# Kernel tuning notes

Hardware: AMD Instinct MI355X
Metric: run time of the kernel (lower is better)

The kernel has to match this reference:

```python
import jax, jax.numpy as jnp
import numpy as np

# Llama-7B-like decode-step config (GQA)
H = 32      # query heads
HKV = 8     # kv heads
D = 128     # head dim
HID = 4096  # hidden size (= H*D)
S = 32768   # stored quantized cache length
B = 1       # batch
Q = 1       # q_len (fused SmartKV path requires q_len == 1)


def rotate_half(x):
    return jnp.concatenate([-x[..., D // 2:], x[..., :D // 2]], axis=-1)


def setup_inputs() -> dict:
    key = jax.random.key(0)
    ks = jax.random.split(key, 9)
    hidden_states = jax.random.normal(ks[0], (B, Q, HID), jnp.float32)
    # quantized KV cache: signed int codes + per-(token, kv_head) scales
    k_qx = jax.random.randint(ks[1], (S, HKV, D), -128, 128, jnp.int32)
    v_qx = jax.random.randint(ks[2], (S, HKV, D), -128, 128, jnp.int32)
    k_scale = jax.random.uniform(ks[3], (S, HKV, 1), jnp.float32, 0.005, 0.02)
    v_scale = jax.random.uniform(ks[4], (S, HKV, 1), jnp.float32, 0.005, 0.02)
    # RoPE angles for the current decode position (pos = S)
    inv_freq = 1.0 / (10000.0 ** (jnp.arange(0, D, 2).astype(jnp.float32) / D))
    ang = jnp.concatenate([S * inv_freq, S * inv_freq])  # [D]
    cos = jnp.cos(ang)
    sin = jnp.sin(ang)
    sc = 1.0 / np.sqrt(HID)
    Wq = jax.random.normal(ks[5], (HID, H * D), jnp.float32) * sc
    Wk = jax.random.normal(ks[6], (HID, HKV * D), jnp.float32) * sc
    Wv = jax.random.normal(ks[7], (HID, HKV * D), jnp.float32) * sc
    Wo = jax.random.normal(ks[8], (H * D, HID), jnp.float32) * sc
    return dict(hidden_states=hidden_states, k_qx=k_qx, k_scale=k_scale,
                v_qx=v_qx, v_scale=v_scale, cos=cos, sin=sin,
                Wq=Wq, Wk=Wk, Wv=Wv, Wo=Wo)


def reference(hidden_states, k_qx, k_scale, v_qx, v_scale, cos, sin, Wq, Wk, Wv, Wo):
    b, q_len, _ = hidden_states.shape  # b=1, q_len=1 (decode)
    G = H // HKV  # GQA group size
    # QKV projections
    q = (hidden_states @ Wq).reshape(b, q_len, H, D).transpose(0, 2, 1, 3)      # [B,H,Q,D]
    k = (hidden_states @ Wk).reshape(b, q_len, HKV, D).transpose(0, 2, 1, 3)    # [B,HKV,Q,D]
    v = (hidden_states @ Wv).reshape(b, q_len, HKV, D).transpose(0, 2, 1, 3)    # [B,HKV,Q,D]
    # RoPE on current-token q, k
    c = cos[None, None, None, :]
    s = sin[None, None, None, :]
    q = q * c + rotate_half(q) * s
    k = k * c + rotate_half(k) * s
    # inline dequantization of SmartKV cache (kept at HKV heads; GQA handled in einsum
    # instead of materializing repeat_interleave)
    Kp = k_qx.astype(jnp.float32) * k_scale  # [S,HKV,D]
    Vp = v_qx.astype(jnp.float32) * v_scale  # [S,HKV,D]
    qg = q.reshape(b, HKV, G, q_len, D)
    scale = 1.0 / jnp.sqrt(jnp.float32(D))
    s_past = jnp.einsum('bkgqd,skd->bkgqs', qg, Kp) * scale        # [B,HKV,G,Q,S]
    s_cur = jnp.einsum('bkgqd,bkqd->bkgq', qg, k)[..., None] * scale  # current token
    scores = jnp.concatenate([s_past, s_cur], axis=-1)             # [B,HKV,G,Q,S+1]
    probs = jax.nn.softmax(scores, axis=-1)
    out = (jnp.einsum('bkgqs,skd->bkgqd', probs[..., :S], Vp)
           + probs[..., S:] * v[:, :, None, :, :])                 # [B,HKV,G,Q,D]
    out = out.reshape(b, H, q_len, D).transpose(0, 2, 1, 3).reshape(b, q_len, H * D)
    return out @ Wo
```

## Files before the change

### kernel.cpp

```cpp
#include <hip/hip_runtime.h>
#include <hip/hip_bf16.h>

#define H_    32
#define HKV_  8
#define D_    128
#define HID_  4096
#define NQKV  6144
#define SPLIT 128
#define CHUNK 256
#define S_    32768
#define NCHUNK (S_ / CHUNK)
#define SCALE_ 0.08838834764831843f
#define BASE_  8.0f

#define WS_QKV_PART 0
#define WS_QKV      786432
#define WS_PV_C     792576
#define WS_L_C      1316864
#define WS_ATTN     1320960
#define WS_OPART    1325056

__global__ __launch_bounds__(256) void k_qkv_part(
    const float* __restrict__ hid, const float* __restrict__ Wq,
    const float* __restrict__ Wk, const float* __restrict__ Wv,
    float* __restrict__ part)
{
    const int j0 = blockIdx.x * 1024 + threadIdx.x * 4;
    const int i0 = blockIdx.y * (HID_ / SPLIT);
    __shared__ float hs[HID_ / SPLIT];
    if (threadIdx.x < HID_ / SPLIT) hs[threadIdx.x] = hid[i0 + threadIdx.x];
    __syncthreads();

    const float* W; int ldw; int col;
    if (j0 < 4096)       { W = Wq; ldw = 4096; col = j0; }
    else if (j0 < 5120)  { W = Wk; ldw = 1024; col = j0 - 4096; }
    else                 { W = Wv; ldw = 1024; col = j0 - 5120; }

    float4 acc = {0.f, 0.f, 0.f, 0.f};
    const float* p = W + (size_t)i0 * ldw + col;
    #pragma unroll 8
    for (int i = 0; i < HID_ / SPLIT; ++i) {
        const float4 wv = *(const float4*)(p + (size_t)i * ldw);
        const float h = hs[i];
        acc.x += h * wv.x; acc.y += h * wv.y; acc.z += h * wv.z; acc.w += h * wv.w;
    }
    *(float4*)&part[(size_t)blockIdx.y * NQKV + j0] = acc;
}

__global__ __launch_bounds__(256) void k_qkv_reduce(
    const float* __restrict__ part, const float* __restrict__ cosv,
    const float* __restrict__ sinv, float* __restrict__ qkv)
{
    const int j = blockIdx.x * 256 + threadIdx.x;
    float s = 0.f;
    #pragma unroll 8
    for (int k = 0; k < SPLIT; ++k) s += part[(size_t)k * NQKV + j];
    __shared__ float buf[256];
    buf[threadIdx.x] = s;
    __syncthreads();
    float out = s;
    if (j < 5120) {
        const int d = j & 127;
        const float rot = (d < 64) ? -buf[threadIdx.x + 64] : buf[threadIdx.x - 64];
        out = s * cosv[d] + rot * sinv[d];
    }
    qkv[j] = out;
}

__global__ __launch_bounds__(256) void k_attn(
    const int* __restrict__ kqx, const float* __restrict__ kscale,
    const int* __restrict__ vqx, const float* __restrict__ vscale,
    const float* __restrict__ qkv, float* __restrict__ pv_c,
    float* __restrict__ l_c)
{
    const int kh = blockIdx.y;
    const int c0 = blockIdx.x * CHUNK;
    const int tid = threadIdx.x;
    const int g = tid >> 6;
    const int l = tid & 63;
    const int t = l >> 3, j = l & 7;

    float4 qf[4];
    #pragma unroll
    for (int k = 0; k < 4; ++k)
        qf[k] = *(const float4*)&qkv[(kh * 4 + g) * D_ + (j + 8 * k) * 4];

    float ls = 0.f;
    float4 acc[4];
    #pragma unroll
    for (int k = 0; k < 4; ++k) acc[k] = make_float4(0.f, 0.f, 0.f, 0.f);

    #pragma unroll 2
    for (int it = 0; it < CHUNK / 8; ++it) {
        const int tok = c0 + it * 8 + t;
        const size_t row = ((size_t)tok * HKV_ + kh) * D_;
        int4 kv[4], vv[4];
        #pragma unroll
        for (int k = 0; k < 4; ++k) kv[k] = *(const int4*)(kqx + row + (j + 8 * k) * 4);
        #pragma unroll
        for (int k = 0; k < 4; ++k) vv[k] = *(const int4*)(vqx + row + (j + 8 * k) * 4);
        const float sc = kscale[tok * HKV_ + kh] * SCALE_;
        const float vs = vscale[tok * HKV_ + kh];

        float dot = 0.f;
        #pragma unroll
        for (int k = 0; k < 4; ++k)
            dot += (float)kv[k].x * qf[k].x + (float)kv[k].y * qf[k].y +
                   (float)kv[k].z * qf[k].z + (float)kv[k].w * qf[k].w;
        dot += __shfl_xor(dot, 1, 64);
        dot += __shfl_xor(dot, 2, 64);
        dot += __shfl_xor(dot, 4, 64);

        const float wgt = __expf(dot * sc - BASE_);
        ls += wgt;
        const float wv = wgt * vs;
        #pragma unroll
        for (int k = 0; k < 4; ++k) {
            acc[k].x += wv * (float)vv[k].x;
            acc[k].y += wv * (float)vv[k].y;
            acc[k].z += wv * (float)vv[k].z;
            acc[k].w += wv * (float)vv[k].w;
        }
    }

    #pragma unroll
    for (int msk = 8; msk < 64; msk <<= 1) {
        #pragma unroll
        for (int k = 0; k < 4; ++k) {
            acc[k].x += __shfl_xor(acc[k].x, msk, 64);
            acc[k].y += __shfl_xor(acc[k].y, msk, 64);
            acc[k].z += __shfl_xor(acc[k].z, msk, 64);
            acc[k].w += __shfl_xor(acc[k].w, msk, 64);
        }
        ls += __shfl_xor(ls, msk, 64);
    }
    if (t == 0) {
        float* dst = pv_c + ((size_t)(blockIdx.x * HKV_ + kh) * 4 + g) * D_;
        #pragma unroll
        for (int k = 0; k < 4; ++k) *(float4*)(dst + (j + 8 * k) * 4) = acc[k];
        if (j == 0) l_c[(blockIdx.x * HKV_ + kh) * 4 + g] = ls;
    }
}

__global__ __launch_bounds__(128) void k_combine(
    const float* __restrict__ pv_c, const float* __restrict__ l_c,
    const float* __restrict__ qkv, float* __restrict__ attn)
{
    const int h = blockIdx.x;
    const int d = threadIdx.x;
    const int kh = h >> 2, g = h & 3;

    __shared__ float sred[128];
    sred[d] = qkv[h * D_ + d] * qkv[4096 + kh * D_ + d];
    __syncthreads();
    for (int s2 = 64; s2 > 0; s2 >>= 1) {
        if (d < s2) sred[d] += sred[d + s2];
        __syncthreads();
    }
    const float pc = __expf(sred[0] * SCALE_ - BASE_);

    float pv = 0.f, dsum = 0.f;
    for (int c = 0; c < NCHUNK; ++c) {
        pv   += pv_c[((size_t)(c * HKV_ + kh) * 4 + g) * D_ + d];
        dsum += l_c[(c * HKV_ + kh) * 4 + g];
    }
    const float vcur = qkv[5120 + kh * D_ + d];
    attn[h * D_ + d] = (pv + pc * vcur) / (dsum + pc);
}

__global__ __launch_bounds__(256) void k_out_part(
    const float* __restrict__ attn, const float* __restrict__ Wo,
    float* __restrict__ opart)
{
    const int j0 = blockIdx.x * 1024 + threadIdx.x * 4;
    const int i0 = blockIdx.y * (HID_ / SPLIT);
    __shared__ float hs[HID_ / SPLIT];
    if (threadIdx.x < HID_ / SPLIT) hs[threadIdx.x] = attn[i0 + threadIdx.x];
    __syncthreads();
    float4 acc = {0.f, 0.f, 0.f, 0.f};
    const float* p = Wo + (size_t)i0 * HID_ + j0;
    #pragma unroll 8
    for (int i = 0; i < HID_ / SPLIT; ++i) {
        const float4 wv = *(const float4*)(p + (size_t)i * HID_);
        const float h = hs[i];
        acc.x += h * wv.x; acc.y += h * wv.y; acc.z += h * wv.z; acc.w += h * wv.w;
    }
    *(float4*)&opart[(size_t)blockIdx.y * HID_ + j0] = acc;
}

__global__ __launch_bounds__(256) void k_out_reduce(
    const float* __restrict__ opart, float* __restrict__ out)
{
    const int j = blockIdx.x * 256 + threadIdx.x;
    float s = 0.f;
    #pragma unroll 8
    for (int k = 0; k < SPLIT; ++k) s += opart[(size_t)k * HID_ + j];
    out[j] = s;
}

extern "C" void kernel_launch(void* const* d_in, const int* in_sizes, int n_in,
                              void* d_out, int out_size, void* d_ws, size_t ws_size,
                              hipStream_t stream) {
    const float* hid    = (const float*)d_in[0];
    const int*   kqx    = (const int*)d_in[1];
    const float* kscale = (const float*)d_in[2];
    const int*   vqx    = (const int*)d_in[3];
    const float* vscale = (const float*)d_in[4];
    const float* cosv   = (const float*)d_in[5];
    const float* sinv   = (const float*)d_in[6];
    const float* Wq     = (const float*)d_in[7];
    const float* Wk     = (const float*)d_in[8];
    const float* Wv     = (const float*)d_in[9];
    const float* Wo     = (const float*)d_in[10];
    float* ws  = (float*)d_ws;
    float* out = (float*)d_out;

    k_qkv_part  <<<dim3(6, SPLIT), 256, 0, stream>>>(hid, Wq, Wk, Wv, ws + WS_QKV_PART);
    k_qkv_reduce<<<dim3(24),       256, 0, stream>>>(ws + WS_QKV_PART, cosv, sinv, ws + WS_QKV);
    k_attn      <<<dim3(NCHUNK, HKV_), 256, 0, stream>>>(kqx, kscale, vqx, vscale,
                                                         ws + WS_QKV, ws + WS_PV_C,
                                                         ws + WS_L_C);
    k_combine   <<<dim3(H_),       128, 0, stream>>>(ws + WS_PV_C, ws + WS_L_C,
                                                     ws + WS_QKV, ws + WS_ATTN);
    k_out_part  <<<dim3(4, SPLIT), 256, 0, stream>>>(ws + WS_ATTN, Wo, ws + WS_OPART);
    k_out_reduce<<<dim3(16),       256, 0, stream>>>(ws + WS_OPART, out);
}
```

Baseline: 137.6 us.

## Stage K/V tiles into LDS with async double-buffered loads shared across GQA heads

In the attention kernel, K/V codes and scales now go through shared memory. A 16-token tile is fetched with global_load_lds direct-to-LDS loads into a double buffer, with an XOR swizzle to avoid bank conflicts. Before, each of the four waves, one per query head in the GQA group, loaded the same K/V rows from global memory on its own. The shared copy is meant to remove that redundant global traffic and overlap the next tile's loads with compute. In exchange it adds LDS usage, a block-wide barrier per tile, and relies on the async loads completing before that barrier.

```diff
diff --git a/kernel.cpp b/kernel.cpp
--- a/kernel.cpp
+++ b/kernel.cpp
@@ -8,10 +8,19 @@
 #define NQKV  6144
 #define SPLIT 128
 #define CHUNK 256
+#define TB    16
+#define NT    (CHUNK / TB)
 #define S_    32768
 #define NCHUNK (S_ / CHUNK)
 #define SCALE_ 0.08838834764831843f
 #define BASE_  8.0f
+
+#define GLOAD_LDS16(g, l) __builtin_amdgcn_global_load_lds( \
+    (const __attribute__((address_space(1))) void*)(g),     \
+    (__attribute__((address_space(3))) void*)(l), 16, 0, 0)
+#define GLOAD_LDS4(g, l) __builtin_amdgcn_global_load_lds(  \
+    (const __attribute__((address_space(1))) void*)(g),     \
+    (__attribute__((address_space(3))) void*)(l), 4, 0, 0)
 
 #define WS_QKV_PART 0
 #define WS_QKV      786432
@@ -80,6 +89,10 @@
     const int l = tid & 63;
     const int t = l >> 3, j = l & 7;
 
+    __shared__ int   kbuf[2][TB * 128];
+    __shared__ int   vbuf[2][TB * 128];
+    __shared__ float scbuf[2][64];
+
     float4 qf[4];
     #pragma unroll
     for (int k = 0; k < 4; ++k)
@@ -90,37 +103,67 @@
     #pragma unroll
     for (int k = 0; k < 4; ++k) acc[k] = make_float4(0.f, 0.f, 0.f, 0.f);
 
-    #pragma unroll 2
-    for (int it = 0; it < CHUNK / 8; ++it) {
-        const int tok = c0 + it * 8 + t;
-        const size_t row = ((size_t)tok * HKV_ + kh) * D_;
-        int4 kv[4], vv[4];
-        #pragma unroll
-        for (int k = 0; k < 4; ++k) kv[k] = *(const int4*)(kqx + row + (j + 8 * k) * 4);
-        #pragma unroll
-        for (int k = 0; k < 4; ++k) vv[k] = *(const int4*)(vqx + row + (j + 8 * k) * 4);
-        const float sc = kscale[tok * HKV_ + kh] * SCALE_;
-        const float vs = vscale[tok * HKV_ + kh];
-
-        float dot = 0.f;
-        #pragma unroll
-        for (int k = 0; k < 4; ++k)
-            dot += (float)kv[k].x * qf[k].x + (float)kv[k].y * qf[k].y +
-                   (float)kv[k].z * qf[k].z + (float)kv[k].w * qf[k].w;
-        dot += __shfl_xor(dot, 1, 64);
-        dot += __shfl_xor(dot, 2, 64);
-        dot += __shfl_xor(dot, 4, 64);
-
-        const float wgt = __expf(dot * sc - BASE_);
-        ls += wgt;
-        const float wv = wgt * vs;
-        #pragma unroll
-        for (int k = 0; k < 4; ++k) {
-            acc[k].x += wv * (float)vv[k].x;
-            acc[k].y += wv * (float)vv[k].y;
-            acc[k].z += wv * (float)vv[k].z;
-            acc[k].w += wv * (float)vv[k].w;
-        }
+    auto stage = [&](int buf, int tok0) {
+        #pragma unroll
+        for (int i = 0; i < 2; ++i) {
+            const int seg = g * 4 + i * 2;
+            const int row = seg + (l >> 5);
+            const int col = ((l & 31) * 16) ^ ((row & 3) << 7);
+            const size_t goff = ((size_t)(tok0 + row) * HKV_ + kh) * D_ + (col >> 2);
+            GLOAD_LDS16(kqx + goff, (char*)&kbuf[buf][0] + seg * 512);
+            GLOAD_LDS16(vqx + goff, (char*)&vbuf[buf][0] + seg * 512);
+        }
+        if (g == 0) {
+            const float* gs;
+            if (l < 16)      gs = kscale + (size_t)(tok0 + l) * HKV_ + kh;
+            else if (l < 32) gs = vscale + (size_t)(tok0 + (l - 16)) * HKV_ + kh;
+            else             gs = kscale + (size_t)tok0 * HKV_ + kh;
+            GLOAD_LDS4(gs, (char*)&scbuf[buf][0]);
+        }
+    };
+
+    stage(0, c0);
+    __syncthreads();
+
+    for (int tile = 0; tile < NT; ++tile) {
+        if (tile + 1 < NT) stage((tile + 1) & 1, c0 + (tile + 1) * TB);
+
+        const int buf = tile & 1;
+        #pragma unroll
+        for (int it = 0; it < TB / 8; ++it) {
+            const int row = it * 8 + t;
+            const int sw = (row & 3) << 7;
+            int4 kv[4], vv[4];
+            #pragma unroll
+            for (int k = 0; k < 4; ++k) {
+                const int off = row * 512 + (((j + 8 * k) * 16) ^ sw);
+                kv[k] = *(const int4*)((const char*)&kbuf[buf][0] + off);
+                vv[k] = *(const int4*)((const char*)&vbuf[buf][0] + off);
+            }
+            const float sc = scbuf[buf][row] * SCALE_;
+            const float vs = scbuf[buf][16 + row];
+
+            float dot = 0.f;
+            #pragma unroll
+            for (int k = 0; k < 4; ++k)
+                dot += (float)kv[k].x * qf[k].x + (float)kv[k].y * qf[k].y +
+                       (float)kv[k].z * qf[k].z + (float)kv[k].w * qf[k].w;
+            dot += __shfl_xor(dot, 1, 64);
+            dot += __shfl_xor(dot, 2, 64);
+            dot += __shfl_xor(dot, 4, 64);
+
+            const float wgt = __expf(dot * sc - BASE_);
+            ls += wgt;
+            const float wv = wgt * vs;
+            #pragma unroll
+            for (int k = 0; k < 4; ++k) {
+                acc[k].x += wv * (float)vv[k].x;
+                acc[k].y += wv * (float)vv[k].y;
+                acc[k].z += wv * (float)vv[k].z;
+                acc[k].w += wv * (float)vv[k].w;
+            }
+        }
+        __syncthreads();
     }
 
     #pragma unroll
```

After: 120.3 us. 12.6% less time.
